# Kernel tuning notes

Hardware: AMD Instinct MI355X
Metric: run time of the kernel (lower is better)

Reference implementation:

```python
import jax, jax.numpy as jnp
import numpy as np

N, M, E, F = 50000, 5000, 200000, 256  # nodes, hyperedges, incidences, channels


def setup_inputs() -> dict:
    key = jax.random.key(0)
    ks = jax.random.split(key, 7)
    x = jax.random.normal(ks[0], (N, F), dtype=jnp.float32)
    hyperedge_attr = jax.random.normal(ks[1], (M, F), dtype=jnp.float32)
    # glorot-ish scale for learned params
    weight = jax.random.normal(ks[2], (F, F), dtype=jnp.float32) * (1.0 / np.sqrt(F))
    att = jax.random.normal(ks[3], (2 * F,), dtype=jnp.float32) * 0.05
    bias = jnp.zeros((F,), dtype=jnp.float32)
    node_idx = jax.random.randint(ks[4], (E,), 0, N)  # hyperedge_index[0]
    edge_idx = jax.random.randint(ks[5], (E,), 0, M)  # hyperedge_index[1]
    return {"x": x, "hyperedge_attr": hyperedge_attr, "weight": weight,
            "att": att, "bias": bias, "node_idx": node_idx, "edge_idx": edge_idx}


def reference(x, hyperedge_attr, weight, att, bias, node_idx, edge_idx):
    # HypergraphConv.forward with use_attention=True, heads=1, concat=True,
    # hyperedge_weight=None (ones), EW_weight=None, dropout=0 (eval).
    n_nodes, feat = x.shape
    n_edges = hyperedge_attr.shape[0]

    he = hyperedge_attr @ weight                       # (M, F)

    # per-incidence attention score: (cat[x_i, he_j] * att).sum(-1)
    alpha = x[node_idx] @ att[:feat] + he[edge_idx] @ att[feat:]   # (E,)
    alpha = jax.nn.leaky_relu(alpha, 0.2)
    # segment softmax over source nodes (hyperedge_index[0])
    amax = jax.lax.stop_gradient(
        jax.ops.segment_max(alpha, node_idx, num_segments=n_nodes))
    ex = jnp.exp(alpha - amax[node_idx])
    denom = jax.ops.segment_sum(ex, node_idx, num_segments=n_nodes)
    alpha = ex / denom[node_idx]                       # (E,)

    ones_e = jnp.ones((node_idx.shape[0],), dtype=x.dtype)
    # D: node degree (hyperedge_weight==1); B: hyperedge cardinality
    D = jax.ops.segment_sum(ones_e, node_idx, num_segments=n_nodes)
    Dinv = jnp.where(D > 0, 1.0 / D, 0.0)
    B = jax.ops.segment_sum(ones_e, edge_idx, num_segments=n_edges)
    Binv = jnp.where(B > 0, 1.0 / B, 0.0)

    # propagate node -> hyperedge: msg = B_i * alpha * x_j, scatter_add at edge
    msg1 = (Binv[edge_idx] * alpha)[:, None] * x[node_idx]          # (E, F)
    edge_out = jax.ops.segment_sum(msg1, edge_idx, num_segments=n_edges)  # (M, F)

    # propagate hyperedge -> node: msg = D_i * alpha * e_j, scatter_add at node
    msg2 = (Dinv[node_idx] * alpha)[:, None] * edge_out[edge_idx]   # (E, F)
    node_out = jax.ops.segment_sum(msg2, node_idx, num_segments=n_nodes)  # (N, F)

    return jax.nn.leaky_relu(node_out + bias, 0.01)
```

## Files before the change

### kernel.cpp

```cpp
#include <hip/hip_runtime.h>
#include <math.h>

#define F 256
#define NODE_STRIDE 32
#define EDGE_STRIDE 128
#define RD_BLOCKS 1792

typedef float f32x4 __attribute__((ext_vector_type(4)));
typedef unsigned short u16x8 __attribute__((ext_vector_type(8)));

__device__ __forceinline__ unsigned short f2bf(float f) {
    unsigned u = __float_as_uint(f);
    u = (u + 0x7FFFu + ((u >> 16) & 1u)) >> 16;
    return (unsigned short)u;
}
__device__ __forceinline__ float bf2f(unsigned short b) {
    return __uint_as_float((unsigned)b << 16);
}

__global__ void k_init_w2(const float* __restrict__ weight, const float* __restrict__ att,
                          float* __restrict__ w2,
                          float* denom, int* npos, int* epos, int N, int M) {
    int b = blockIdx.x, t = threadIdx.x;
    if (b < 64) {
        int wid = t >> 6, lane = t & 63;
        int row = b * 4 + wid;
        float4 wr = ((const float4*)(weight + (size_t)row * F))[lane];
        float4 av = ((const float4*)(att + F))[lane];
        float s = wr.x * av.x + wr.y * av.y + wr.z * av.z + wr.w * av.w;
        #pragma unroll
        for (int o = 32; o >= 1; o >>= 1) s += __shfl_down(s, o, 64);
        if (lane == 0) w2[row] = s;
    } else {
        int total = N > M ? N : M;
        int nth = (gridDim.x - 64) * blockDim.x;
        for (int i = (b - 64) * blockDim.x + t; i < total; i += nth) {
            if (i < N) { denom[i] = 0.0f; npos[i] = 0; }
            if (i < M) { epos[i] = 0; }
        }
    }
}

__global__ void k_rowdot(const float* __restrict__ x, const float* __restrict__ attr,
                         const float* __restrict__ att, const float* __restrict__ w2,
                         float* __restrict__ xa, float* __restrict__ hea,
                         unsigned short* __restrict__ xb,
                         int N, int M) {
    int gw   = (blockIdx.x * blockDim.x + threadIdx.x) >> 6;
    int lane = threadIdx.x & 63;
    const int nw = (RD_BLOCKS * 256) >> 6;
    const int rows = N + M;
    float4 av = ((const float4*)att)[lane];
    float4 wv = ((const float4*)w2)[lane];

    for (int rb = gw; rb < rows; rb += 4 * nw) {
        int   r[4]; bool val[4]; float s[4];
        float4 rv[4];
        #pragma unroll
        for (int k = 0; k < 4; ++k) {
            r[k]   = rb + k * nw;
            val[k] = r[k] < rows;
            const float* src = (r[k] < N) ? x + (size_t)r[k] * F
                     : attr + (size_t)(val[k] ? r[k] - N : 0) * F;
            rv[k] = val[k] ? ((const float4*)src)[lane]
                           : make_float4(0.f, 0.f, 0.f, 0.f);
        }
        #pragma unroll
        for (int k = 0; k < 4; ++k) {
            if (val[k] && r[k] < N) {
                ushort4 c;
                c.x = f2bf(rv[k].x); c.y = f2bf(rv[k].y);
                c.z = f2bf(rv[k].z); c.w = f2bf(rv[k].w);
                ((ushort4*)(xb + (size_t)r[k] * F))[lane] = c;
            }
            float4 vv = (r[k] < N) ? av : wv;
            s[k] = rv[k].x * vv.x + rv[k].y * vv.y + rv[k].z * vv.z + rv[k].w * vv.w;
        }
        #pragma unroll
        for (int o = 32; o >= 1; o >>= 1) {
            s[0] += __shfl_down(s[0], o, 64);
            s[1] += __shfl_down(s[1], o, 64);
            s[2] += __shfl_down(s[2], o, 64);
            s[3] += __shfl_down(s[3], o, 64);
        }
        if (lane == 0) {
            #pragma unroll
            for (int k = 0; k < 4; ++k) {
                if (val[k]) {
                    if (r[k] < N) xa[r[k]] = s[k];
                    else          hea[r[k] - N] = s[k];
                }
            }
        }
    }
}

__global__ void k_alpha_scatter(const float* __restrict__ xa, const float* __restrict__ hea,
                                const int* __restrict__ node_idx, const int* __restrict__ edge_idx,
                                float* denom, int* npos, int* epos,
                                int2* __restrict__ node_pairs, int2* __restrict__ edge_pairs,
                                int E) {
    int i = blockIdx.x * blockDim.x + threadIdx.x;
    int E4 = E >> 2;
    if (i < E4) {
        int4 nn = ((const int4*)node_idx)[i];
        int4 mm = ((const int4*)edge_idx)[i];
        float a0 = xa[nn.x] + hea[mm.x];
        float a1 = xa[nn.y] + hea[mm.y];
        float a2 = xa[nn.z] + hea[mm.z];
        float a3 = xa[nn.w] + hea[mm.w];
        a0 = a0 > 0.f ? a0 : 0.2f * a0;
        a1 = a1 > 0.f ? a1 : 0.2f * a1;
        a2 = a2 > 0.f ? a2 : 0.2f * a2;
        a3 = a3 > 0.f ? a3 : 0.2f * a3;
        float e0 = expf(a0), e1 = expf(a1), e2 = expf(a2), e3 = expf(a3);
        atomicAdd(&denom[nn.x], e0); atomicAdd(&denom[nn.y], e1);
        atomicAdd(&denom[nn.z], e2); atomicAdd(&denom[nn.w], e3);
        int p;
        p = atomicAdd(&npos[nn.x], 1); if (p < NODE_STRIDE) node_pairs[(size_t)nn.x * NODE_STRIDE + p] = make_int2(mm.x, __float_as_int(e0));
        p = atomicAdd(&npos[nn.y], 1); if (p < NODE_STRIDE) node_pairs[(size_t)nn.y * NODE_STRIDE + p] = make_int2(mm.y, __float_as_int(e1));
        p = atomicAdd(&npos[nn.z], 1); if (p < NODE_STRIDE) node_pairs[(size_t)nn.z * NODE_STRIDE + p] = make_int2(mm.z, __float_as_int(e2));
        p = atomicAdd(&npos[nn.w], 1); if (p < NODE_STRIDE) node_pairs[(size_t)nn.w * NODE_STRIDE + p] = make_int2(mm.w, __float_as_int(e3));
        p = atomicAdd(&epos[mm.x], 1); if (p < EDGE_STRIDE) edge_pairs[(size_t)mm.x * EDGE_STRIDE + p] = make_int2(nn.x, __float_as_int(e0));
        p = atomicAdd(&epos[mm.y], 1); if (p < EDGE_STRIDE) edge_pairs[(size_t)mm.y * EDGE_STRIDE + p] = make_int2(nn.y, __float_as_int(e1));
        p = atomicAdd(&epos[mm.z], 1); if (p < EDGE_STRIDE) edge_pairs[(size_t)mm.z * EDGE_STRIDE + p] = make_int2(nn.z, __float_as_int(e2));
        p = atomicAdd(&epos[mm.w], 1); if (p < EDGE_STRIDE) edge_pairs[(size_t)mm.w * EDGE_STRIDE + p] = make_int2(nn.w, __float_as_int(e3));
    } else if (i == E4) {
        for (int e = E4 * 4; e < E; ++e) {
            int n = node_idx[e], m = edge_idx[e];
            float a = xa[n] + hea[m];
            a = a > 0.f ? a : 0.2f * a;
            float ex = expf(a);
            atomicAdd(&denom[n], ex);
            int p = atomicAdd(&npos[n], 1);
            if (p < NODE_STRIDE) node_pairs[(size_t)n * NODE_STRIDE + p] = make_int2(m, __float_as_int(ex));
            int q = atomicAdd(&epos[m], 1);
            if (q < EDGE_STRIDE) edge_pairs[(size_t)m * EDGE_STRIDE + q] = make_int2(n, __float_as_int(ex));
        }
    }
}

__global__ void k_edge_gather(const unsigned short* __restrict__ xb,
                              const float* __restrict__ denom,
                              const int2* __restrict__ edge_pairs,
                              const int* __restrict__ epos,
                              unsigned short* __restrict__ edge_out, int M) {
    int wid = threadIdx.x >> 6, lane = threadIdx.x & 63;
    int half = lane >> 5, fl = lane & 31;
    int nwaves = gridDim.x * 4;
    for (int m = blockIdx.x * 4 + wid; m < M; m += nwaves) {
        int B = epos[m];
        int cnt = B < EDGE_STRIDE ? B : EDGE_STRIDE;
        const int2* pairs = edge_pairs + (size_t)m * EDGE_STRIDE;
        float acc[8] = {0.f, 0.f, 0.f, 0.f, 0.f, 0.f, 0.f, 0.f};
        for (int base = half * 16; base < cnt; base += 32) {
            int li = base + (fl & 15);
            int2 pl = pairs[li < cnt ? li : cnt - 1];
            float wl = __int_as_float(pl.y) / denom[pl.x];
            int rem = cnt - base; if (rem > 16) rem = 16;
            #pragma unroll
            for (int j = 0; j < 16; ++j) {
                if (j < rem) {
                    int   nj = __shfl(pl.x, j, 32);
                    float wj = __shfl(wl,   j, 32);
                    u16x8 v = ((const u16x8*)(xb + (size_t)nj * F))[fl];
                    #pragma unroll
                    for (int q = 0; q < 8; ++q) acc[q] += wj * bf2f(v[q]);
                }
            }
        }
        #pragma unroll
        for (int q = 0; q < 8; ++q) acc[q] += __shfl_xor(acc[q], 32, 64);
        if (half == 0) {
            float Binv = (B > 0) ? 1.0f / (float)B : 0.0f;
            u16x8 r;
            #pragma unroll
            for (int q = 0; q < 8; ++q) r[q] = f2bf(acc[q] * Binv);
            ((u16x8*)(edge_out + (size_t)m * F))[fl] = r;
        }
    }
}

__global__ void k_node_gather(const unsigned short* __restrict__ edge_out,
                              const int2* __restrict__ node_pairs,
                              const float* __restrict__ bias,
                              const int* __restrict__ npos,
                              const float* __restrict__ denom,
                              float* __restrict__ out, int N) {
    int wid = threadIdx.x >> 6, lane = threadIdx.x & 63;
    int half = lane >> 5, fl = lane & 31;
    f32x4 b0 = ((const f32x4*)bias)[fl * 2];
    f32x4 b1 = ((const f32x4*)bias)[fl * 2 + 1];
    int nhalves = gridDim.x * 8;
    for (int n = blockIdx.x * 8 + wid * 2 + half; n < N; n += nhalves) {
        int D = npos[n];
        int cnt = D < NODE_STRIDE ? D : NODE_STRIDE;
        const int2* pairs = node_pairs + (size_t)n * NODE_STRIDE;
        float acc[8] = {0.f, 0.f, 0.f, 0.f, 0.f, 0.f, 0.f, 0.f};
        for (int base = 0; base < cnt; base += 16) {
            int li = base + (fl & 15);
            int2 pl = pairs[li < cnt ? li : cnt - 1];
            float wl = __int_as_float(pl.y);
            int rem = cnt - base; if (rem > 16) rem = 16;
            #pragma unroll
            for (int j = 0; j < 16; ++j) {
                if (j < rem) {
                    int   mj = __shfl(pl.x, j, 32);
                    float wj = __shfl(wl,   j, 32);
                    u16x8 v = ((const u16x8*)(edge_out + (size_t)mj * F))[fl];
                    #pragma unroll
                    for (int q = 0; q < 8; ++q) acc[q] += wj * bf2f(v[q]);
                }
            }
        }
        float scale = (D > 0) ? 1.0f / ((float)D * denom[n]) : 0.0f;
        f32x4 r0, r1;
        r0.x = acc[0] * scale + b0.x; r0.y = acc[1] * scale + b0.y;
        r0.z = acc[2] * scale + b0.z; r0.w = acc[3] * scale + b0.w;
        r1.x = acc[4] * scale + b1.x; r1.y = acc[5] * scale + b1.y;
        r1.z = acc[6] * scale + b1.z; r1.w = acc[7] * scale + b1.w;
        r0.x = r0.x > 0.f ? r0.x : 0.01f * r0.x;
        r0.y = r0.y > 0.f ? r0.y : 0.01f * r0.y;
        r0.z = r0.z > 0.f ? r0.z : 0.01f * r0.z;
        r0.w = r0.w > 0.f ? r0.w : 0.01f * r0.w;
        r1.x = r1.x > 0.f ? r1.x : 0.01f * r1.x;
        r1.y = r1.y > 0.f ? r1.y : 0.01f * r1.y;
        r1.z = r1.z > 0.f ? r1.z : 0.01f * r1.z;
        r1.w = r1.w > 0.f ? r1.w : 0.01f * r1.w;
        __builtin_nontemporal_store(r0, (f32x4*)(out + (size_t)n * F) + fl * 2);
        __builtin_nontemporal_store(r1, (f32x4*)(out + (size_t)n * F) + fl * 2 + 1);
    }
}

extern "C" void kernel_launch(void* const* d_in, const int* in_sizes, int n_in,
                              void* d_out, int out_size, void* d_ws, size_t ws_size,
                              hipStream_t stream) {
    const float* x        = (const float*)d_in[0];
    const float* attr     = (const float*)d_in[1];
    const float* weight   = (const float*)d_in[2];
    const float* att      = (const float*)d_in[3];
    const float* bias     = (const float*)d_in[4];
    const int*   node_idx = (const int*)d_in[5];
    const int*   edge_idx = (const int*)d_in[6];

    const int Fdim = in_sizes[4];
    const int N = in_sizes[0] / Fdim;
    const int M = in_sizes[1] / Fdim;
    const int E = in_sizes[5];
    float* out = (float*)d_out;

    char* ws = (char*)d_ws;
    auto alloc = [&](size_t bytes) -> void* {
        void* p = (void*)ws;
        ws += ((bytes + 255) / 256) * 256;
        return p;
    };
    float*          w2         = (float*)alloc((size_t)Fdim * 4);
    float*          xa         = (float*)alloc((size_t)N * 4);
    float*          hea        = (float*)alloc((size_t)M * 4);
    float*          denom      = (float*)alloc((size_t)N * 4);
    int*            npos       = (int*)alloc((size_t)N * 4);
    int*            epos       = (int*)alloc((size_t)M * 4);
    unsigned short* xb         = (unsigned short*)alloc((size_t)N * Fdim * 2);
    int2*           node_pairs = (int2*)alloc((size_t)N * NODE_STRIDE * 8);
    int2*           edge_pairs = (int2*)alloc((size_t)M * EDGE_STRIDE * 8);
    unsigned short* edge_out   = (unsigned short*)alloc((size_t)M * Fdim * 2);

    hipLaunchKernelGGL(k_init_w2, dim3(256), dim3(256), 0, stream,
                       weight, att, w2, denom, npos, epos, N, M);
    hipLaunchKernelGGL(k_rowdot, dim3(RD_BLOCKS), dim3(256), 0, stream,
                       x, attr, att, w2, xa, hea, xb, N, M);
    int E4 = E / 4;
    hipLaunchKernelGGL(k_alpha_scatter, dim3((E4 + 1 + 255) / 256), dim3(256), 0, stream,
                       xa, hea, node_idx, edge_idx, denom, npos, epos,
                       node_pairs, edge_pairs, E);
    int egrid = (M + 3) / 4;
    hipLaunchKernelGGL(k_edge_gather, dim3(egrid), dim3(256), 0, stream,
                       xb, denom, edge_pairs, epos, edge_out, M);
    hipLaunchKernelGGL(k_node_gather, dim3(2048), dim3(256), 0, stream,
                       edge_out, node_pairs, bias, npos, denom, out, N);
}
```

Before: 97.43 us.

## Pack node count and fixed-point softmax denom into one 64-bit atomic

Replaces the separate float denom atomicAdd and int npos atomicAdd per incidence with a single 64-bit atomicAdd. The count sits in the top 16 bits and the exp value, quantized to 16.16 fixed point, in the low bits. This halves node-side atomics and merges two arrays into one read in the gather kernels. It also moves workspace zeroing from the init kernel into extra blocks of the rowdot kernel, and processes two incidences per thread instead of four. Fixed-point quantization adds rounding error to the denominator, and the low field could overflow into the count bits if the exp sums get large.

Result: faster. 87.91 us, median of 2 (-9.8%).

```diff
diff --git a/kernel.cpp b/kernel.cpp
--- a/kernel.cpp
+++ b/kernel.cpp
@@ -4,7 +4,9 @@
 #define F 256
 #define NODE_STRIDE 32
 #define EDGE_STRIDE 128
+#define ZB 64
 #define RD_BLOCKS 1792
+#define Q16 65536.0f
 
 typedef float f32x4 __attribute__((ext_vector_type(4)));
 typedef unsigned short u16x8 __attribute__((ext_vector_type(8)));
@@ -19,35 +21,32 @@
 }
 
 __global__ void k_init_w2(const float* __restrict__ weight, const float* __restrict__ att,
-                          float* __restrict__ w2,
-                          float* denom, int* npos, int* epos, int N, int M) {
-    int b = blockIdx.x, t = threadIdx.x;
-    if (b < 64) {
-        int wid = t >> 6, lane = t & 63;
-        int row = b * 4 + wid;
-        float4 wr = ((const float4*)(weight + (size_t)row * F))[lane];
-        float4 av = ((const float4*)(att + F))[lane];
-        float s = wr.x * av.x + wr.y * av.y + wr.z * av.z + wr.w * av.w;
-        #pragma unroll
-        for (int o = 32; o >= 1; o >>= 1) s += __shfl_down(s, o, 64);
-        if (lane == 0) w2[row] = s;
-    } else {
-        int total = N > M ? N : M;
-        int nth = (gridDim.x - 64) * blockDim.x;
-        for (int i = (b - 64) * blockDim.x + t; i < total; i += nth) {
-            if (i < N) { denom[i] = 0.0f; npos[i] = 0; }
-            if (i < M) { epos[i] = 0; }
-        }
-    }
+                          float* __restrict__ w2) {
+    int wid = threadIdx.x >> 6, lane = threadIdx.x & 63;
+    int row = blockIdx.x * 4 + wid;
+    float4 wr = ((const float4*)(weight + (size_t)row * F))[lane];
+    float4 av = ((const float4*)(att + F))[lane];
+    float s = wr.x * av.x + wr.y * av.y + wr.z * av.z + wr.w * av.w;
+    #pragma unroll
+    for (int o = 32; o >= 1; o >>= 1) s += __shfl_down(s, o, 64);
+    if (lane == 0) w2[row] = s;
 }
 
 __global__ void k_rowdot(const float* __restrict__ x, const float* __restrict__ attr,
                          const float* __restrict__ att, const float* __restrict__ w2,
                          float* __restrict__ xa, float* __restrict__ hea,
                          unsigned short* __restrict__ xb,
+                         unsigned long long* packed, int* epos,
                          int N, int M) {
-    int gw   = (blockIdx.x * blockDim.x + threadIdx.x) >> 6;
-    int lane = threadIdx.x & 63;
+    int b = blockIdx.x, t = threadIdx.x;
+    if (b < ZB) {
+        int nth = ZB * 256;
+        for (int i = b * 256 + t; i < N; i += nth) packed[i] = 0ULL;
+        for (int i = b * 256 + t; i < M; i += nth) epos[i] = 0;
+        return;
+    }
+    int gw   = ((b - ZB) * 256 + t) >> 6;
+    int lane = t & 63;
     const int nw = (RD_BLOCKS * 256) >> 6;
     const int rows = N + M;
     float4 av = ((const float4*)att)[lane];
@@ -97,57 +96,54 @@
 
 __global__ void k_alpha_scatter(const float* __restrict__ xa, const float* __restrict__ hea,
                                 const int* __restrict__ node_idx, const int* __restrict__ edge_idx,
-                                float* denom, int* npos, int* epos,
+                                unsigned long long* packed, int* epos,
                                 int2* __restrict__ node_pairs, int2* __restrict__ edge_pairs,
                                 int E) {
     int i = blockIdx.x * blockDim.x + threadIdx.x;
-    int E4 = E >> 2;
-    if (i < E4) {
-        int4 nn = ((const int4*)node_idx)[i];
-        int4 mm = ((const int4*)edge_idx)[i];
+    int E2 = E >> 1;
+    if (i < E2) {
+        int2 nn = ((const int2*)node_idx)[i];
+        int2 mm = ((const int2*)edge_idx)[i];
         float a0 = xa[nn.x] + hea[mm.x];
         float a1 = xa[nn.y] + hea[mm.y];
-        float a2 = xa[nn.z] + hea[mm.z];
-        float a3 = xa[nn.w] + hea[mm.w];
         a0 = a0 > 0.f ? a0 : 0.2f * a0;
         a1 = a1 > 0.f ? a1 : 0.2f * a1;
-        a2 = a2 > 0.f ? a2 : 0.2f * a2;
-        a3 = a3 > 0.f ? a3 : 0.2f * a3;
-        float e0 = expf(a0), e1 = expf(a1), e2 = expf(a2), e3 = expf(a3);
-        atomicAdd(&denom[nn.x], e0); atomicAdd(&denom[nn.y], e1);
-        atomicAdd(&denom[nn.z], e2); atomicAdd(&denom[nn.w], e3);
-        int p;
-        p = atomicAdd(&npos[nn.x], 1); if (p < NODE_STRIDE) node_pairs[(size_t)nn.x * NODE_STRIDE + p] = make_int2(mm.x, __float_as_int(e0));
-        p = atomicAdd(&npos[nn.y], 1); if (p < NODE_STRIDE) node_pairs[(size_t)nn.y * NODE_STRIDE + p] = make_int2(mm.y, __float_as_int(e1));
-        p = atomicAdd(&npos[nn.z], 1); if (p < NODE_STRIDE) node_pairs[(size_t)nn.z * NODE_STRIDE + p] = make_int2(mm.z, __float_as_int(e2));
-        p = atomicAdd(&npos[nn.w], 1); if (p < NODE_STRIDE) node_pairs[(size_t)nn.w * NODE_STRIDE + p] = make_int2(mm.w, __float_as_int(e3));
-        p = atomicAdd(&epos[mm.x], 1); if (p < EDGE_STRIDE) edge_pairs[(size_t)mm.x * EDGE_STRIDE + p] = make_int2(nn.x, __float_as_int(e0));
-        p = atomicAdd(&epos[mm.y], 1); if (p < EDGE_STRIDE) edge_pairs[(size_t)mm.y * EDGE_STRIDE + p] = make_int2(nn.y, __float_as_int(e1));
-        p = atomicAdd(&epos[mm.z], 1); if (p < EDGE_STRIDE) edge_pairs[(size_t)mm.z * EDGE_STRIDE + p] = make_int2(nn.z, __float_as_int(e2));
-        p = atomicAdd(&epos[mm.w], 1); if (p < EDGE_STRIDE) edge_pairs[(size_t)mm.w * EDGE_STRIDE + p] = make_int2(nn.w, __float_as_int(e3));
-    } else if (i == E4) {
-        for (int e = E4 * 4; e < E; ++e) {
-            int n = node_idx[e], m = edge_idx[e];
-            float a = xa[n] + hea[m];
-            a = a > 0.f ? a : 0.2f * a;
-            float ex = expf(a);
-            atomicAdd(&denom[n], ex);
-            int p = atomicAdd(&npos[n], 1);
-            if (p < NODE_STRIDE) node_pairs[(size_t)n * NODE_STRIDE + p] = make_int2(m, __float_as_int(ex));
-            int q = atomicAdd(&epos[m], 1);
-            if (q < EDGE_STRIDE) edge_pairs[(size_t)m * EDGE_STRIDE + q] = make_int2(n, __float_as_int(ex));
-        }
+        float e0 = expf(a0), e1 = expf(a1);
+        unsigned long long inc0 = (1ULL << 48) | (unsigned long long)__float2uint_rn(e0 * Q16);
+        unsigned long long inc1 = (1ULL << 48) | (unsigned long long)__float2uint_rn(e1 * Q16);
+        unsigned long long o0 = atomicAdd(&packed[nn.x], inc0);
+        unsigned long long o1 = atomicAdd(&packed[nn.y], inc1);
+        int p0 = (int)(o0 >> 48);
+        int p1 = (int)(o1 >> 48);
+        if (p0 < NODE_STRIDE) node_pairs[(size_t)nn.x * NODE_STRIDE + p0] = make_int2(mm.x, __float_as_int(e0));
+        if (p1 < NODE_STRIDE) node_pairs[(size_t)nn.y * NODE_STRIDE + p1] = make_int2(mm.y, __float_as_int(e1));
+        int q0 = atomicAdd(&epos[mm.x], 1);
+        int q1 = atomicAdd(&epos[mm.y], 1);
+        if (q0 < EDGE_STRIDE) edge_pairs[(size_t)mm.x * EDGE_STRIDE + q0] = make_int2(nn.x, __float_as_int(e0));
+        if (q1 < EDGE_STRIDE) edge_pairs[(size_t)mm.y * EDGE_STRIDE + q1] = make_int2(nn.y, __float_as_int(e1));
+    } else if (i == E2 && (E & 1)) {
+        int n = node_idx[E - 1], m = edge_idx[E - 1];
+        float a = xa[n] + hea[m];
+        a = a > 0.f ? a : 0.2f * a;
+        float ex = expf(a);
+        unsigned long long o = atomicAdd(&packed[n],
+            (1ULL << 48) | (unsigned long long)__float2uint_rn(ex * Q16));
+        int p = (int)(o >> 48);
+        if (p < NODE_STRIDE) node_pairs[(size_t)n * NODE_STRIDE + p] = make_int2(m, __float_as_int(ex));
+        int q = atomicAdd(&epos[m], 1);
+        if (q < EDGE_STRIDE) edge_pairs[(size_t)m * EDGE_STRIDE + q] = make_int2(n, __float_as_int(ex));
     }
 }
 
 __global__ void k_edge_gather(const unsigned short* __restrict__ xb,
-                              const float* __restrict__ denom,
+                              const unsigned long long* __restrict__ packed,
                               const int2* __restrict__ edge_pairs,
                               const int* __restrict__ epos,
                               unsigned short* __restrict__ edge_out, int M) {
     int wid = threadIdx.x >> 6, lane = threadIdx.x & 63;
     int half = lane >> 5, fl = lane & 31;
     int nwaves = gridDim.x * 4;
+    const unsigned* packedLo = (const unsigned*)packed;
     for (int m = blockIdx.x * 4 + wid; m < M; m += nwaves) {
         int B = epos[m];
         int cnt = B < EDGE_STRIDE ? B : EDGE_STRIDE;
@@ -156,7 +152,8 @@
         for (int base = half * 16; base < cnt; base += 32) {
             int li = base + (fl & 15);
             int2 pl = pairs[li < cnt ? li : cnt - 1];
-            float wl = __int_as_float(pl.y) / denom[pl.x];
+            unsigned dq = packedLo[(size_t)pl.x << 1];
+            float wl = __int_as_float(pl.y) * (Q16 / (float)dq);
             int rem = cnt - base; if (rem > 16) rem = 16;
             #pragma unroll
             for (int j = 0; j < 16; ++j) {
@@ -184,8 +181,7 @@
 __global__ void k_node_gather(const unsigned short* __restrict__ edge_out,
                               const int2* __restrict__ node_pairs,
                               const float* __restrict__ bias,
-                              const int* __restrict__ npos,
-                              const float* __restrict__ denom,
+                              const unsigned long long* __restrict__ packed,
                               float* __restrict__ out, int N) {
     int wid = threadIdx.x >> 6, lane = threadIdx.x & 63;
     int half = lane >> 5, fl = lane & 31;
@@ -193,8 +189,10 @@
     f32x4 b1 = ((const f32x4*)bias)[fl * 2 + 1];
     int nhalves = gridDim.x * 8;
     for (int n = blockIdx.x * 8 + wid * 2 + half; n < N; n += nhalves) {
-        int D = npos[n];
-        int cnt = D < NODE_STRIDE ? D : NODE_STRIDE;
+        unsigned long long pk = packed[n];
+        unsigned D  = (unsigned)(pk >> 48);
+        unsigned dq = (unsigned)pk;
+        int cnt = (int)D < NODE_STRIDE ? (int)D : NODE_STRIDE;
         const int2* pairs = node_pairs + (size_t)n * NODE_STRIDE;
         float acc[8] = {0.f, 0.f, 0.f, 0.f, 0.f, 0.f, 0.f, 0.f};
         for (int base = 0; base < cnt; base += 16) {
@@ -213,7 +211,7 @@
                 }
             }
         }
-        float scale = (D > 0) ? 1.0f / ((float)D * denom[n]) : 0.0f;
+        float scale = (D > 0) ? Q16 / ((float)D * (float)dq) : 0.0f;
         f32x4 r0, r1;
         r0.x = acc[0] * scale + b0.x; r0.y = acc[1] * scale + b0.y;
         r0.z = acc[2] * scale + b0.z; r0.w = acc[3] * scale + b0.w;
@@ -255,28 +253,26 @@
         ws += ((bytes + 255) / 256) * 256;
         return p;
     };
-    float*          w2         = (float*)alloc((size_t)Fdim * 4);
-    float*          xa         = (float*)alloc((size_t)N * 4);
-    float*          hea        = (float*)alloc((size_t)M * 4);
-    float*          denom      = (float*)alloc((size_t)N * 4);
-    int*            npos       = (int*)alloc((size_t)N * 4);
-    int*            epos       = (int*)alloc((size_t)M * 4);
-    unsigned short* xb         = (unsigned short*)alloc((size_t)N * Fdim * 2);
-    int2*           node_pairs = (int2*)alloc((size_t)N * NODE_STRIDE * 8);
-    int2*           edge_pairs = (int2*)alloc((size_t)M * EDGE_STRIDE * 8);
-    unsigned short* edge_out   = (unsigned short*)alloc((size_t)M * Fdim * 2);
-
-    hipLaunchKernelGGL(k_init_w2, dim3(256), dim3(256), 0, stream,
-                       weight, att, w2, denom, npos, epos, N, M);
-    hipLaunchKernelGGL(k_rowdot, dim3(RD_BLOCKS), dim3(256), 0, stream,
-                       x, attr, att, w2, xa, hea, xb, N, M);
-    int E4 = E / 4;
-    hipLaunchKernelGGL(k_alpha_scatter, dim3((E4 + 1 + 255) / 256), dim3(256), 0, stream,
-                       xa, hea, node_idx, edge_idx, denom, npos, epos,
+    float*              w2         = (float*)alloc((size_t)Fdim * 4);
+    float*              xa         = (float*)alloc((size_t)N * 4);
+    float*              hea        = (float*)alloc((size_t)M * 4);
+    unsigned long long* packed     = (unsigned long long*)alloc((size_t)N * 8);
+    int*                epos       = (int*)alloc((size_t)M * 4);
+    unsigned short*     xb         = (unsigned short*)alloc((size_t)N * Fdim * 2);
+    int2*               node_pairs = (int2*)alloc((size_t)N * NODE_STRIDE * 8);
+    int2*               edge_pairs = (int2*)alloc((size_t)M * EDGE_STRIDE * 8);
+    unsigned short*     edge_out   = (unsigned short*)alloc((size_t)M * Fdim * 2);
+
+    hipLaunchKernelGGL(k_init_w2, dim3(64), dim3(256), 0, stream, weight, att, w2);
+    hipLaunchKernelGGL(k_rowdot, dim3(ZB + RD_BLOCKS), dim3(256), 0, stream,
+                       x, attr, att, w2, xa, hea, xb, packed, epos, N, M);
+    int E2 = E / 2;
+    hipLaunchKernelGGL(k_alpha_scatter, dim3((E2 + 1 + 255) / 256), dim3(256), 0, stream,
+                       xa, hea, node_idx, edge_idx, packed, epos,
                        node_pairs, edge_pairs, E);
     int egrid = (M + 3) / 4;
     hipLaunchKernelGGL(k_edge_gather, dim3(egrid), dim3(256), 0, stream,
-                       xb, denom, edge_pairs, epos, edge_out, M);
+                       xb, packed, edge_pairs, epos, edge_out, M);
     hipLaunchKernelGGL(k_node_gather, dim3(2048), dim3(256), 0, stream,
-                       edge_out, node_pairs, bias, npos, denom, out, N);
-}
+                       edge_out, node_pairs, bias, packed, out, N);
+}
```
